# Optimization experiments

Hardware: AMD Instinct MI355X
Metric: run time of the kernel (lower is better)

## Reference

```python
import jax, jax.numpy as jnp
import numpy as np

B, T, F, H = 256, 512, 128, 256


def setup_inputs() -> dict:
    key = jax.random.key(0)
    k1, k2, k3, k4 = jax.random.split(key, 4)
    return {
        "x": jax.random.normal(k1, (B, T, F), dtype=jnp.float32),
        "kernel": jax.random.normal(k2, (F, 3 * H), dtype=jnp.float32) * 0.05,
        "recurrent_kernel": jax.random.normal(k3, (H, 3 * H), dtype=jnp.float32) * 0.05,
        "bias": jax.random.normal(k4, (2, 3 * H), dtype=jnp.float32) * 0.05,
    }


def reference(x, kernel, recurrent_kernel, bias):
    # Keras GRUCell with reset_after=True (TF2 default):
    #   matrix_x = x @ kernel + input_bias     -> split z, r, h
    #   matrix_h = h @ rec_kernel + rec_bias   -> split z, r, h
    #   z = sigmoid(xz+hz); r = sigmoid(xr+hr)
    #   c = tanh(xh + r * hh_inner);  h_new = z*h + (1-z)*c
    input_bias, rec_bias = bias[0], bias[1]
    batch = x.shape[0]
    hid = recurrent_kernel.shape[0]

    def step(h, xt):
        mx = xt @ kernel + input_bias            # (B, 3H)
        mh = h @ recurrent_kernel + rec_bias     # (B, 3H)
        xz, xr, xh = jnp.split(mx, 3, axis=-1)
        hz, hr, hh = jnp.split(mh, 3, axis=-1)
        z = jax.nn.sigmoid(xz + hz)
        r = jax.nn.sigmoid(xr + hr)
        c = jnp.tanh(xh + r * hh)
        h_new = z * h + (1.0 - z) * c
        return h_new, h_new

    h0 = jnp.zeros((batch, hid), dtype=x.dtype)
    xt = jnp.swapaxes(x, 0, 1)  # (T, B, F)
    _, states = jax.lax.scan(step, h0, xt)
    return states  # (T, B, H): all per-step hidden states, matching X1..XT
```

## Files before the change

kernel.cpp:

```cpp
#include <hip/hip_runtime.h>
#include <cstdint>
#include <cstddef>


typedef _Float16 half8 __attribute__((ext_vector_type(8)));
typedef float floatx4 __attribute__((ext_vector_type(4)));

#define RPACK_OFF   0
#define WKPACK_OFF  393216
#define BIASP_OFF   589824
#define MXP_OFF     1048576

#define NLOG2E  (-1.4426950408889634f)
#define N2LOG2E (-2.8853900817779268f)

#if defined(__has_builtin)
#if __has_builtin(__builtin_amdgcn_rcpf)
#define RCPF(x) __builtin_amdgcn_rcpf(x)
#else
#define RCPF(x) (1.0f/(x))
#endif
#if __has_builtin(__builtin_amdgcn_exp2f)
#define EXP2F(x) __builtin_amdgcn_exp2f(x)
#else
#define EXP2F(x) exp2f(x)
#endif
#else
#define RCPF(x) (1.0f/(x))
#define EXP2F(x) exp2f(x)
#endif

__device__ __forceinline__ int jt_of(int w, int s) {
    return (s < 2) ? (2 * w + s) : (s < 4) ? (16 + 2 * w + (s - 2)) : (32 + 2 * w + (s - 4));
}

__global__ void k0_pack(const float* __restrict__ Wk, const float* __restrict__ Rk,
                        const float* __restrict__ bias, char* __restrict__ ws) {
    int tid = blockIdx.x * 256 + threadIdx.x;
    _Float16* Rp = (_Float16*)(ws + RPACK_OFF);
    _Float16* Wp = (_Float16*)(ws + WKPACK_OFF);
    float* bp = (float*)(ws + BIASP_OFF);
    if (tid < 24576) {
        int l = tid & 63, kt = (tid >> 6) & 7, jt = tid >> 9;
        int col = jt * 16 + (l & 15);
        float sc = (col < 512) ? NLOG2E : N2LOG2E;
        int k0 = kt * 32 + (l >> 4) * 8;
        half8 v;
#pragma unroll
        for (int i = 0; i < 8; ++i) v[i] = (_Float16)(sc * Rk[(k0 + i) * 768 + col]);
        *(half8*)(Rp + (size_t)tid * 8) = v;
    } else if (tid < 36864) {
        int j = tid - 24576;
        int l = j & 63, kt = (j >> 6) & 3, jt = j >> 8;
        int col = jt * 16 + (l & 15);
        float sc = (col < 512) ? NLOG2E : N2LOG2E;
        int k0 = kt * 32 + (l >> 4) * 8;
        half8 v;
#pragma unroll
        for (int i = 0; i < 8; ++i) v[i] = (_Float16)(sc * Wk[(k0 + i) * 768 + col]);
        *(half8*)(Wp + (size_t)j * 8) = v;
    } else if (tid < 37632) {
        int c = tid - 36864;
        bp[c] = (c < 512) ? NLOG2E * (bias[c] + bias[768 + c])
                          : N2LOG2E * bias[c];
    }
}

__launch_bounds__(512, 2)
__global__ void k1_mx(const float* __restrict__ x, char* __restrict__ ws) {
    __shared__ __attribute__((aligned(16))) char xl[8192];
    int bid = blockIdx.x;
    int t = bid >> 3, jp = bid & 7;
    int b0 = jp * 32;
    int tid = threadIdx.x;
    int l = tid & 63, w = tid >> 6;
    int l15 = l & 15, hi = l >> 4;
    const _Float16* Wp = (const _Float16*)(ws + WKPACK_OFF);
    const float* bp = (const float*)(ws + BIASP_OFF);
    _Float16* MXp = (_Float16*)(ws + MXP_OFF);

    {
        int rid = tid >> 4, f8 = (tid & 15) * 8;
        const float* src = x + ((size_t)(b0 + rid) * 512 + (size_t)t) * 128 + f8;
        floatx4 v0 = *(const floatx4*)src;
        floatx4 v1 = *(const floatx4*)(src + 4);
        half8 h;
#pragma unroll
        for (int i = 0; i < 4; ++i) { h[i] = (_Float16)v0[i]; h[4 + i] = (_Float16)v1[i]; }
        int byte = (rid * 256 + f8 * 2) ^ ((rid & 7) << 4);
        *(half8*)(xl + byte) = h;
    }

    half8 wk[6][4];
    floatx4 acA[6], acB[6];
#pragma unroll
    for (int s = 0; s < 6; ++s) {
        int jt = jt_of(w, s);
#pragma unroll
        for (int kt = 0; kt < 4; ++kt)
            wk[s][kt] = *(const half8*)(Wp + ((size_t)(jt * 4 + kt) * 64 + l) * 8);
        float bv = bp[jt * 16 + l15];
        acA[s] = (floatx4){bv, bv, bv, bv};
        acB[s] = (floatx4){bv, bv, bv, bv};
    }
    __syncthreads();

    int hi16 = hi * 16;
#pragma unroll
    for (int kt = 0; kt < 4; ++kt) {
        int r0 = l15, r1 = 16 + l15;
        half8 a0 = *(const half8*)(xl + r0 * 256 + ((kt * 64 + hi16) ^ ((r0 & 7) << 4)));
        half8 a1 = *(const half8*)(xl + r1 * 256 + ((kt * 64 + hi16) ^ ((r1 & 7) << 4)));
#pragma unroll
        for (int s = 0; s < 6; ++s) {
            acA[s] = __builtin_amdgcn_mfma_f32_16x16x32_f16(a0, wk[s][kt], acA[s], 0, 0, 0);
            acB[s] = __builtin_amdgcn_mfma_f32_16x16x32_f16(a1, wk[s][kt], acB[s], 0, 0, 0);
        }
    }

    int g0 = (t * 16 + jp * 2) * 8 + w;
#pragma unroll
    for (int i = 0; i < 3; ++i) {
        half8 h0, h1;
#pragma unroll
        for (int q = 0; q < 4; ++q) {
            h0[q] = (_Float16)acA[2 * i][q]; h0[4 + q] = (_Float16)acA[2 * i + 1][q];
            h1[q] = (_Float16)acB[2 * i][q]; h1[4 + q] = (_Float16)acB[2 * i + 1][q];
        }
        *(half8*)(MXp + ((size_t)(g0 * 3 + i) * 64 + l) * 8) = h0;
        *(half8*)(MXp + ((size_t)((g0 + 8) * 3 + i) * 64 + l) * 8) = h1;
    }
}

#define MFMA6(A, KT) do { \
    ac0 = __builtin_amdgcn_mfma_f32_16x16x32_f16((A), bf[0][KT], ac0, 0, 0, 0); \
    ac1 = __builtin_amdgcn_mfma_f32_16x16x32_f16((A), bf[1][KT], ac1, 0, 0, 0); \
    ac2 = __builtin_amdgcn_mfma_f32_16x16x32_f16((A), bf[2][KT], ac2, 0, 0, 0); \
    ac3 = __builtin_amdgcn_mfma_f32_16x16x32_f16((A), bf[3][KT], ac3, 0, 0, 0); \
    ac4 = __builtin_amdgcn_mfma_f32_16x16x32_f16((A), bf[4][KT], ac4, 0, 0, 0); \
    ac5 = __builtin_amdgcn_mfma_f32_16x16x32_f16((A), bf[5][KT], ac5, 0, 0, 0); \
} while (0)

__launch_bounds__(512, 1)
__global__ void k2_rec(const float* __restrict__ biasraw, const char* __restrict__ ws,
                       float* __restrict__ out) {
    __shared__ __attribute__((aligned(16))) char hl[16384];
    int nb = blockIdx.x;
    int tid = threadIdx.x;
    int l = tid & 63, w = tid >> 6;
    int l15 = l & 15, hi = l >> 4;
    const _Float16* Rp = (const _Float16*)(ws + RPACK_OFF);

    half8 bf[6][8];
#pragma unroll
    for (int s = 0; s < 6; ++s) {
        int jt = jt_of(w, s);
#pragma unroll
        for (int kt = 0; kt < 8; ++kt)
            bf[s][kt] = *(const half8*)(Rp + ((size_t)(jt * 8 + kt) * 64 + l) * 8);
    }
    float brh0 = N2LOG2E * biasraw[768 + 512 + 32 * w + l15];
    float brh1 = N2LOG2E * biasraw[768 + 512 + 32 * w + l15 + 16];

    *(floatx4*)(hl + tid * 16) = (floatx4){0.f, 0.f, 0.f, 0.f};
    float h0q[4] = {0.f, 0.f, 0.f, 0.f}, h1q[4] = {0.f, 0.f, 0.f, 0.f};

    const int arow = l15 * 512;
    const int asw = (l15 & 7) << 4;
    const int hi16 = hi * 16;
#define ARD(KT) (*(const half8*)(hr + (((KT) * 64 + hi16) ^ asw)))

    const int ca2 = (32 * w + l15) * 2;
    const int cb2 = (32 * w + 16 + l15) * 2;

    const char* mxp = (const char*)(ws + MXP_OFF) + (size_t)(nb * 8 + w) * 3072 + (size_t)l * 16;
    half8 m0 = *(const half8*)(mxp);
    half8 m1 = *(const half8*)(mxp + 1024);
    half8 m2 = *(const half8*)(mxp + 2048);

    float* outp = out + (size_t)(nb * 16 + hi * 4) * 256 + 32 * w + l15;

    __syncthreads();

    int rb = 0;
    for (int t = 0; t < 512; ++t) {
        const char* hr = hl + rb + arow;
        half8 a0 = ARD(0), a1 = ARD(1), a2 = ARD(2), a3 = ARD(3);

        floatx4 ac0, ac1, ac2, ac3, ac4, ac5;
#pragma unroll
        for (int q = 0; q < 4; ++q) {
            ac0[q] = (float)m0[q];     ac1[q] = (float)m0[4 + q];
            ac2[q] = (float)m1[q];     ac3[q] = (float)m1[4 + q];
        }
        ac4 = (floatx4){brh0, brh0, brh0, brh0};
        ac5 = (floatx4){brh1, brh1, brh1, brh1};

        const char* mxn = mxp + (size_t)(t < 511 ? t + 1 : t) * 393216;
        m0 = *(const half8*)(mxn);
        m1 = *(const half8*)(mxn + 1024);
        half8 m2n = *(const half8*)(mxn + 2048);
        if (t) {
            size_t tp = (size_t)(t - 1) * 65536;
#pragma unroll
            for (int q = 0; q < 4; ++q) {
                outp[tp + q * 256] = h0q[q];
                outp[tp + q * 256 + 16] = h1q[q];
            }
        }

        MFMA6(a0, 0); a0 = ARD(4);
        MFMA6(a1, 1); a1 = ARD(5);
        MFMA6(a2, 2); a2 = ARD(6);
        MFMA6(a3, 3); a3 = ARD(7);
        MFMA6(a0, 4);
        MFMA6(a1, 5);
        MFMA6(a2, 6);
        MFMA6(a3, 7);

        char* hw_ = hl + (rb ^ 8192);
#pragma unroll
        for (int q = 0; q < 4; ++q) {
            float z0 = RCPF(1.0f + EXP2F(ac0[q]));
            float r0 = RCPF(1.0f + EXP2F(ac2[q]));
            float y0 = (float)m2[q] + r0 * ac4[q];
            float c0 = __builtin_fmaf(2.0f, RCPF(1.0f + EXP2F(y0)), -1.0f);
            float hn0 = __builtin_fmaf(z0, h0q[q] - c0, c0);
            h0q[q] = hn0;
            float z1 = RCPF(1.0f + EXP2F(ac1[q]));
            float r1 = RCPF(1.0f + EXP2F(ac3[q]));
            float y1 = (float)m2[4 + q] + r1 * ac5[q];
            float c1 = __builtin_fmaf(2.0f, RCPF(1.0f + EXP2F(y1)), -1.0f);
            float hn1 = __builtin_fmaf(z1, h1q[q] - c1, c1);
            h1q[q] = hn1;

            int rbase = (4 * hi + q) * 512;
            int sw = ((4 * hi + q) & 7) << 4;
            *(_Float16*)(hw_ + ((rbase + ca2) ^ sw)) = (_Float16)hn0;
            *(_Float16*)(hw_ + ((rbase + cb2) ^ sw)) = (_Float16)hn1;
        }
        m2 = m2n;

        __syncthreads();
        rb ^= 8192;
    }
    size_t tp = (size_t)511 * 65536;
#pragma unroll
    for (int q = 0; q < 4; ++q) {
        outp[tp + q * 256] = h0q[q];
        outp[tp + q * 256 + 16] = h1q[q];
    }
#undef ARD
}

extern "C" void kernel_launch(void* const* d_in, const int* in_sizes, int n_in,
                              void* d_out, int out_size, void* d_ws, size_t ws_size,
                              hipStream_t stream) {
    const float* x    = (const float*)d_in[0];
    const float* Wk   = (const float*)d_in[1];
    const float* Rk   = (const float*)d_in[2];
    const float* bias = (const float*)d_in[3];
    float* out = (float*)d_out;
    char* ws = (char*)d_ws;

    k0_pack<<<147, 256, 0, stream>>>(Wk, Rk, bias, ws);
    k1_mx<<<4096, 512, 0, stream>>>(x, ws);
    k2_rec<<<16, 512, 0, stream>>>(bias, ws, out);
}
```

Before: 1.504 ms.

## Prefetch precomputed input gates into LDS via async global_load_lds double buffer

The recurrent kernel now stages the next timestep's precomputed input-projection tile into a double-buffered LDS region using global_load_lds, instead of holding register prefetches of it. The per-step LDS A-fragment reads drop from four live registers to two rotating ones, and asm barriers pin the recurrent weight fragments in VGPRs. The goal is to cut register pressure and hide global latency on the serial critical path, at the cost of extra LDS traffic and reliance on the barrier to order the async copies.

```diff
diff --git a/kernel.cpp b/kernel.cpp
--- a/kernel.cpp
+++ b/kernel.cpp
@@ -30,6 +30,10 @@
 #define EXP2F(x) exp2f(x)
 #endif
 
+#define GLL16(gp, lp) __builtin_amdgcn_global_load_lds( \
+    (const __attribute__((address_space(1))) void*)(gp), \
+    (__attribute__((address_space(3))) void*)(lp), 16, 0, 0)
+
 __device__ __forceinline__ int jt_of(int w, int s) {
     return (s < 2) ? (2 * w + s) : (s < 4) ? (16 + 2 * w + (s - 2)) : (32 + 2 * w + (s - 4));
 }
@@ -145,6 +149,7 @@
 __global__ void k2_rec(const float* __restrict__ biasraw, const char* __restrict__ ws,
                        float* __restrict__ out) {
     __shared__ __attribute__((aligned(16))) char hl[16384];
+    __shared__ __attribute__((aligned(16))) char mxl[2][24576];
     int nb = blockIdx.x;
     int tid = threadIdx.x;
     int l = tid & 63, w = tid >> 6;
@@ -159,6 +164,12 @@
         for (int kt = 0; kt < 8; ++kt)
             bf[s][kt] = *(const half8*)(Rp + ((size_t)(jt * 8 + kt) * 64 + l) * 8);
     }
+#pragma unroll
+    for (int s = 0; s < 6; ++s)
+#pragma unroll
+        for (int kt = 0; kt < 8; ++kt)
+            asm volatile("" : "+v"(bf[s][kt]));
+
     float brh0 = N2LOG2E * biasraw[768 + 512 + 32 * w + l15];
     float brh1 = N2LOG2E * biasraw[768 + 512 + 32 * w + l15 + 16];
 
@@ -173,19 +184,40 @@
     const int ca2 = (32 * w + l15) * 2;
     const int cb2 = (32 * w + 16 + l15) * 2;
 
-    const char* mxp = (const char*)(ws + MXP_OFF) + (size_t)(nb * 8 + w) * 3072 + (size_t)l * 16;
-    half8 m0 = *(const half8*)(mxp);
-    half8 m1 = *(const half8*)(mxp + 1024);
-    half8 m2 = *(const half8*)(mxp + 2048);
+    const char* mxg = (const char*)(ws + MXP_OFF) + (size_t)(nb * 8 + w) * 3072 + (size_t)l * 16;
+    char* mxdst = mxl[0] + w * 3072;
+    const char* mxrd = mxl[0] + w * 3072 + l * 16;
+
+    GLL16(mxg, mxdst);
+    GLL16(mxg + 1024, mxdst + 1024);
+    GLL16(mxg + 2048, mxdst + 2048);
 
     float* outp = out + (size_t)(nb * 16 + hi * 4) * 256 + 32 * w + l15;
 
     __syncthreads();
 
     int rb = 0;
+    int mb = 0;
     for (int t = 0; t < 512; ++t) {
+        {
+            const char* gq = mxg + (size_t)(t < 511 ? t + 1 : 511) * 393216;
+            char* lq = mxdst + (mb ^ 24576);
+            GLL16(gq, lq);
+            GLL16(gq + 1024, lq + 1024);
+            GLL16(gq + 2048, lq + 2048);
+        }
+        if (t) {
+            float* op = outp + (size_t)(t - 1) * 65536;
+#pragma unroll
+            for (int q = 0; q < 4; ++q) { op[q * 256] = h0q[q]; op[q * 256 + 16] = h1q[q]; }
+        }
+
+        half8 m0 = *(const half8*)(mxrd + mb);
+        half8 m1 = *(const half8*)(mxrd + mb + 1024);
+        half8 m2 = *(const half8*)(mxrd + mb + 2048);
+
         const char* hr = hl + rb + arow;
-        half8 a0 = ARD(0), a1 = ARD(1), a2 = ARD(2), a3 = ARD(3);
+        half8 a0 = ARD(0), a1 = ARD(1);
 
         floatx4 ac0, ac1, ac2, ac3, ac4, ac5;
 #pragma unroll
@@ -196,27 +228,14 @@
         ac4 = (floatx4){brh0, brh0, brh0, brh0};
         ac5 = (floatx4){brh1, brh1, brh1, brh1};
 
-        const char* mxn = mxp + (size_t)(t < 511 ? t + 1 : t) * 393216;
-        m0 = *(const half8*)(mxn);
-        m1 = *(const half8*)(mxn + 1024);
-        half8 m2n = *(const half8*)(mxn + 2048);
-        if (t) {
-            size_t tp = (size_t)(t - 1) * 65536;
-#pragma unroll
-            for (int q = 0; q < 4; ++q) {
-                outp[tp + q * 256] = h0q[q];
-                outp[tp + q * 256 + 16] = h1q[q];
-            }
-        }
-
-        MFMA6(a0, 0); a0 = ARD(4);
-        MFMA6(a1, 1); a1 = ARD(5);
-        MFMA6(a2, 2); a2 = ARD(6);
-        MFMA6(a3, 3); a3 = ARD(7);
-        MFMA6(a0, 4);
-        MFMA6(a1, 5);
-        MFMA6(a2, 6);
-        MFMA6(a3, 7);
+        MFMA6(a0, 0); a0 = ARD(2);
+        MFMA6(a1, 1); a1 = ARD(3);
+        MFMA6(a0, 2); a0 = ARD(4);
+        MFMA6(a1, 3); a1 = ARD(5);
+        MFMA6(a0, 4); a0 = ARD(6);
+        MFMA6(a1, 5); a1 = ARD(7);
+        MFMA6(a0, 6);
+        MFMA6(a1, 7);
 
         char* hw_ = hl + (rb ^ 8192);
 #pragma unroll
@@ -239,16 +258,15 @@
             *(_Float16*)(hw_ + ((rbase + ca2) ^ sw)) = (_Float16)hn0;
             *(_Float16*)(hw_ + ((rbase + cb2) ^ sw)) = (_Float16)hn1;
         }
-        m2 = m2n;
 
         __syncthreads();
         rb ^= 8192;
-    }
-    size_t tp = (size_t)511 * 65536;
-#pragma unroll
-    for (int q = 0; q < 4; ++q) {
-        outp[tp + q * 256] = h0q[q];
-        outp[tp + q * 256 + 16] = h1q[q];
+        mb ^= 24576;
+    }
+    {
+        float* op = outp + (size_t)511 * 65536;
+#pragma unroll
+        for (int q = 0; q < 4; ++q) { op[q * 256] = h0q[q]; op[q * 256 + 16] = h1q[q]; }
     }
 #undef ARD
 }
```

After: 1.512 ms. About the same (+0.5%).
